# Kernel optimization log

Hardware: AMD Instinct MI355X
Metric: run time of the kernel (lower is better)

Reference implementation:

```python
import jax, jax.numpy as jnp
import numpy as np

N_WAY = 2
K_SHOT = 5
C = 320
NPTS = 2048
NQ = 2
K_PROTO = 100  # hardcoded k=100 in forward
N_CLS = N_WAY + 1
SIGMA = 1.0
NEG = -1e9


def _l2norm(x, eps=1e-8):
    return x / (jnp.linalg.norm(x, axis=-1, keepdims=True) + eps)


def _class_prototypes(feat, mask, k):
    """Multi-prototype masked pooling for one class.
    feat: [M, C] point features; mask: [M] float (1 = belongs to class).
    Picks k masked seed points, assigns every masked point to its
    nearest (cosine) seed, and returns the k masked cluster means.
    """
    M = feat.shape[0]
    # deterministic seeds: first k masked points (tie-break by index)
    score = mask - jnp.arange(M, dtype=feat.dtype) * 1e-9
    _, seed_idx = jax.lax.top_k(score, k)
    seeds = feat[seed_idx]                      # [k, C]
    sim = _l2norm(feat) @ _l2norm(seeds).T      # [M, k]
    assign = jnp.argmax(sim, axis=1)            # [M]
    onehot = jax.nn.one_hot(assign, k, dtype=feat.dtype) * mask[:, None]  # [M, k]
    num = onehot.T @ feat                       # [k, C]
    den = onehot.sum(axis=0)[:, None] + 1e-8
    return num / den


def _fg_prototypes(support_feat, fg_mask, k):
    # support_feat [n_way, k_shot, C, N] -> per-class point sets [n_way, k_shot*N, C]
    feat = support_feat.transpose(0, 1, 3, 2).reshape(N_WAY, -1, C)
    m = fg_mask.reshape(N_WAY, -1).astype(feat.dtype)
    protos = jax.vmap(lambda f, mm: _class_prototypes(f, mm, k))(feat, m)  # [n_way, k, C]
    labels = jnp.repeat(jnp.arange(1, N_WAY + 1), k)                        # classes 1..n_way
    return protos.reshape(-1, C), jax.nn.one_hot(labels, N_CLS, dtype=feat.dtype)


def _bg_prototypes(support_feat, bg_mask, k):
    feat = support_feat.transpose(0, 1, 3, 2).reshape(-1, C)   # all shots pooled
    m = bg_mask.reshape(-1).astype(feat.dtype)
    protos = _class_prototypes(feat, m, k)                      # [k, C]
    labels = jnp.zeros((k,), dtype=jnp.int32)                   # class 0 = background
    return protos, jax.nn.one_hot(labels, N_CLS, dtype=feat.dtype)


def _predict(prototypes, proto_onehot, qfeat, qlabels):
    # cosine similarity [M, P], per-class max over that class's prototypes
    sim = (_l2norm(qfeat) @ _l2norm(prototypes).T) / SIGMA        # [M, P]
    cls_mask = proto_onehot.T[None] > 0                            # [1, ncls, P]
    pred = jnp.max(jnp.where(cls_mask, sim[:, None, :], NEG), axis=-1)  # [M, ncls]
    logp = jax.nn.log_softmax(pred, axis=-1)
    loss = -jnp.mean(jnp.take_along_axis(logp, qlabels.reshape(-1, 1), axis=1))
    query_pred = pred.reshape(NQ, NPTS, N_CLS).transpose(0, 2, 1)  # [NQ, ncls, NPTS]
    return loss, query_pred


def reference(support_feat, query_feat, support_y, query_y):
    fg_mask = support_y
    bg_mask = 1 - support_y
    fg_protos, fg_labels = _fg_prototypes(support_feat, fg_mask, K_PROTO)
    bg_protos, bg_labels = _bg_prototypes(support_feat, bg_mask, K_PROTO)
    prototypes = jnp.concatenate([bg_protos, fg_protos], axis=0)           # [P, C]
    proto_labels = jnp.concatenate([bg_labels, fg_labels], axis=0)         # [P, ncls]

    qfeat = query_feat.transpose(0, 2, 1).reshape(-1, C)                   # [NQ*NPTS, C]
    loss, query_pred = _predict(prototypes, proto_labels, qfeat, query_y)
    # the forward adds computeCrossEntropyLoss(query_pred, query_y): same CE again
    loss = loss * 2.0

    # post-hoc per-point confidence thresholding (vectorized Python loop)
    qp = jnp.concatenate([query_pred[0], query_pred[1]], axis=-1)          # [ncls, NQ*NPTS]
    predictions = jnp.argmax(qp, axis=0)
    confidences = jnp.max(qp, axis=0)
    final = jnp.where(confidences > jnp.mean(confidences), predictions, -1)
    final_labels = jnp.stack([final[:NPTS], final[NPTS:]], axis=0)         # [2, NPTS]
    return loss, query_pred, final_labels


def setup_inputs() -> dict:
    key = jax.random.key(0)
    k1, k2, k3, k4 = jax.random.split(key, 4)
    return {
        "support_feat": jax.random.normal(k1, (N_WAY, K_SHOT, C, NPTS), dtype=jnp.float32),
        "query_feat": jax.random.normal(k2, (NQ, C, NPTS), dtype=jnp.float32),
        "support_y": jax.random.randint(k3, (N_WAY, K_SHOT, NPTS), 0, 2, dtype=jnp.int32),
        "query_y": jax.random.randint(k4, (NQ, NPTS), 0, 3, dtype=jnp.int32),
    }
```

## Files before the change

### kernel.cpp

```cpp
#include <hip/hip_runtime.h>
#include <math.h>

#define C 320
#define NPTS 2048
#define SUPPTS 20480
#define QPTS 4096
#define KP 100
#define NCLS 3
#define PSTRIDE 300

__global__ __launch_bounds__(64) void k_protoseed(const float* __restrict__ sup,
                                                  const int* __restrict__ sy,
                                                  float* __restrict__ pbufT) {
    int p    = blockIdx.x;
    int lane = threadIdx.x;
    int prob = (p < 100) ? 2 : ((p < 200) ? 0 : 1);
    int rank = (p < 100) ? p : ((p < 200) ? p - 100 : p - 200);
    int M    = (prob == 2) ? SUPPTS : 10240;
    int base = (prob == 1) ? 10240 : 0;
    int found = 0, sp = 0;
    for (int chunk = 0; chunk < M; chunk += 64) {
        int yy = sy[base + chunk + lane];
        int m  = (prob == 2) ? (1 - yy) : yy;
        unsigned long long bal = __ballot(m != 0);
        int cnt = __popcll(bal);
        if (found + cnt > rank) {
            int need = rank - found;
            int prefix = __popcll(bal & ((1ull << lane) - 1ull));
            unsigned long long match = __ballot(m && (prefix == need));
            int pos = __ffsll((unsigned long long)match) - 1;
            sp = base + chunk + pos;
            break;
        }
        found += cnt;
    }
    const float* fb = sup + ((size_t)(sp >> 11) * C) * NPTS + (sp & 2047);
    float v[5]; float s = 0.f;
    #pragma unroll
    for (int i = 0; i < 5; i++) {
        v[i] = fb[(size_t)(lane + i * 64) * NPTS];
        s += v[i] * v[i];
    }
    #pragma unroll
    for (int off = 32; off > 0; off >>= 1) s += __shfl_down(s, off);
    s = __shfl(s, 0);
    float r = 1.0f / (sqrtf(s) + 1e-8f);
    #pragma unroll
    for (int i = 0; i < 5; i++)
        pbufT[(size_t)(lane + i * 64) * PSTRIDE + p] = v[i] * r;
}

__global__ __launch_bounds__(256) void k_assign(const float* __restrict__ sup,
                                                const int* __restrict__ sy,
                                                const float* __restrict__ pbT,
                                                float* __restrict__ pmaxv,
                                                int* __restrict__ pmaxj) {
    __shared__ float shp[2 * C * 12 + 16];
    int b = blockIdx.x, jt = blockIdx.y, tid = threadIdx.x;
    int w = (b >= 40) ? 1 : 0;
    int colf = 100 + w * 100 + jt * 10;
    int colb = jt * 10;
    const int BGOFF = C * 12 + 16;
    for (int i = tid; i < C * 10; i += 256) {
        int c = i / 10, j = i % 10;
        shp[c * 12 + j]         = pbT[(size_t)c * PSTRIDE + colf + j];
        shp[BGOFF + c * 12 + j] = pbT[(size_t)c * PSTRIDE + colb + j];
    }
    int g = b * 256 + tid;
    int sel = sy[g] ? 0 : BGOFF;
    __syncthreads();
    const float* fb = sup + ((size_t)(g >> 11) * C) * NPTS + (g & 2047);
    float acc[10];
    #pragma unroll
    for (int j = 0; j < 10; j++) acc[j] = 0.f;
    float pf[8];
    #pragma unroll
    for (int k = 0; k < 8; k++) pf[k] = fb[(size_t)k * NPTS];
    for (int cc = 0; cc < C; cc += 8) {
        float cur[8];
        #pragma unroll
        for (int k = 0; k < 8; k++) cur[k] = pf[k];
        if (cc + 8 < C) {
            #pragma unroll
            for (int k = 0; k < 8; k++) pf[k] = fb[(size_t)(cc + 8 + k) * NPTS];
        }
        #pragma unroll
        for (int k = 0; k < 8; k++) {
            const float* row = &shp[sel + (cc + k) * 12];
            float4 p0 = ((const float4*)row)[0];
            float4 p1 = ((const float4*)row)[1];
            float2 p2 = *(const float2*)(row + 8);
            float px = cur[k];
            acc[0] += px * p0.x; acc[1] += px * p0.y;
            acc[2] += px * p0.z; acc[3] += px * p0.w;
            acc[4] += px * p1.x; acc[5] += px * p1.y;
            acc[6] += px * p1.z; acc[7] += px * p1.w;
            acc[8] += px * p2.x; acc[9] += px * p2.y;
        }
    }
    float bv = acc[0]; int bj = 0;
    #pragma unroll
    for (int j = 1; j < 10; j++) {
        if (acc[j] > bv) { bv = acc[j]; bj = j; }
    }
    size_t a0 = (size_t)jt * 20480 + g;
    pmaxv[a0] = bv;
    pmaxj[a0] = jt * 10 + bj;
}

__global__ __launch_bounds__(256) void k_combine_dst(const float* __restrict__ pmaxv,
                                                     const int* __restrict__ pmaxj,
                                                     const int* __restrict__ sy,
                                                     int* __restrict__ dst,
                                                     float* __restrict__ loss) {
    int g = blockIdx.x * 256 + threadIdx.x;
    if (g == 0) loss[0] = 0.f;
    if (g == 1) loss[1] = 0.f;
    float bv = pmaxv[g]; int bj = pmaxj[g];
    #pragma unroll
    for (int t = 1; t < 10; t++) {
        float v = pmaxv[(size_t)t * 20480 + g];
        if (v > bv) { bv = v; bj = pmaxj[(size_t)t * 20480 + g]; }
    }
    int way = (g >= 10240) ? 1 : 0;
    dst[g] = sy[g] ? (100 + way * 100 + bj) : bj;
}

__global__ __launch_bounds__(256) void k_accum_lds(const float* __restrict__ sup,
                                                   const int* __restrict__ dst,
                                                   float* __restrict__ part,
                                                   float* __restrict__ cnt) {
    __shared__ float bins[8 * 800];
    __shared__ float scnt[800];
    int bx = blockIdx.x;
    int ct = blockIdx.y;
    int tid = threadIdx.x;
    int copy = tid & 3;
    int ws = bx >> 1, half = bx & 1;
    int w = (ws >= 5) ? 1 : 0;
    int nbase = half * 1024;
    for (int i = tid; i < 8 * 800; i += 256) bins[i] = 0.f;
    if (ct == 0) { for (int i = tid; i < 800; i += 256) scnt[i] = 0.f; }
    int dreg[4];
    #pragma unroll
    for (int sub = 0; sub < 4; sub++) {
        int d = dst[ws * 2048 + nbase + sub * 256 + tid];
        dreg[sub] = (d < 100) ? d : (d - w * 100);
    }
    __syncthreads();
    if (ct == 0) {
        #pragma unroll
        for (int sub = 0; sub < 4; sub++) atomicAdd(&scnt[copy * 200 + dreg[sub]], 1.0f);
    }
    const float* base = sup + ((size_t)ws * C + ct * 8) * NPTS + nbase;
    for (int cl = 0; cl < 8; cl++) {
        const float* row = base + (size_t)cl * NPTS;
        #pragma unroll
        for (int sub = 0; sub < 4; sub++)
            atomicAdd(&bins[cl * 800 + copy * 200 + dreg[sub]], row[sub * 256 + tid]);
    }
    __syncthreads();
    float* pout = part + (size_t)(bx * 40 + ct) * 1600;
    for (int i = tid; i < 8 * 200; i += 256) {
        int bin = i >> 3, cl = i & 7;
        float s = bins[cl * 800 + bin] + bins[cl * 800 + 200 + bin]
                + bins[cl * 800 + 400 + bin] + bins[cl * 800 + 600 + bin];
        pout[i] = s;
    }
    if (ct == 0 && tid < 200)
        cnt[bx * 200 + tid] = scnt[tid] + scnt[200 + tid] + scnt[400 + tid] + scnt[600 + tid];
}

__global__ __launch_bounds__(64) void k_reduce_proto(const float* __restrict__ part,
                                                     const float* __restrict__ cnt,
                                                     float* __restrict__ phatT) {
    int d   = blockIdx.x;
    int tid = threadIdx.x;
    int local, s0, ns;
    if (d < 100)      { local = d;       s0 = 0;  ns = 20; }
    else if (d < 200) { local = d;       s0 = 0;  ns = 10; }
    else              { local = d - 100; s0 = 10; ns = 10; }
    float dn = 0.f;
    for (int k = 0; k < ns; k++) dn += cnt[(s0 + k) * 200 + local];
    float inv = 1.0f / (dn + 1e-8f);
    float vals[5]; float sq = 0.f;
    #pragma unroll
    for (int i = 0; i < 5; i++) {
        int c = tid + i * 64;
        int ct = c >> 3, cl = c & 7;
        float s = 0.f;
        for (int k = 0; k < ns; k++)
            s += part[(size_t)((s0 + k) * 40 + ct) * 1600 + local * 8 + cl];
        float v = s * inv;
        vals[i] = v; sq += v * v;
    }
    #pragma unroll
    for (int off = 32; off > 0; off >>= 1) sq += __shfl_down(sq, off);
    sq = __shfl(sq, 0);
    float rn = 1.0f / (sqrtf(sq) + 1e-8f);
    #pragma unroll
    for (int i = 0; i < 5; i++)
        phatT[(size_t)(tid + i * 64) * PSTRIDE + d] = vals[i] * rn;
}

__global__ __launch_bounds__(256) void k_qpartial(const float* __restrict__ qry,
                                                  const float* __restrict__ phT,
                                                  float* __restrict__ qmaxv,
                                                  float* __restrict__ qrn) {
    __shared__ float shp[C * 16];
    __shared__ float red[3 * 64 * 45];
    int pb = blockIdx.x, jt = blockIdx.y, tid = threadIdx.x;
    int wave = tid >> 6, lane = tid & 63;
    int j0 = jt * 10;
    for (int i = tid; i < C * 10; i += 256) {
        int j = i % 10, c = i / 10;
        shp[c * 16 + j] = phT[(size_t)c * PSTRIDE + j0 + j];
    }
    __syncthreads();
    int m = pb * 256 + lane * 4;
    int c0 = wave * 80;
    const float* fb = qry + ((size_t)(m >> 11) * C + c0) * NPTS + (m & 2047);
    float acc[4][10];
    #pragma unroll
    for (int p = 0; p < 4; p++)
        #pragma unroll
        for (int j = 0; j < 10; j++) acc[p][j] = 0.f;
    float qn[4] = {0.f, 0.f, 0.f, 0.f};
    float4 pf[8];
    #pragma unroll
    for (int k = 0; k < 8; k++) pf[k] = *(const float4*)(fb + (size_t)k * NPTS);
    for (int cc = 0; cc < 80; cc += 8) {
        float4 cur[8];
        #pragma unroll
        for (int k = 0; k < 8; k++) cur[k] = pf[k];
        if (cc + 8 < 80) {
            #pragma unroll
            for (int k = 0; k < 8; k++) pf[k] = *(const float4*)(fb + (size_t)(cc + 8 + k) * NPTS);
        }
        #pragma unroll
        for (int k = 0; k < 8; k++) {
            const float* row = &shp[(c0 + cc + k) * 16];
            float4 p0 = ((const float4*)row)[0];
            float4 p1 = ((const float4*)row)[1];
            float2 p2 = ((const float2*)row)[4];
            float pr[10] = {p0.x,p0.y,p0.z,p0.w,p1.x,p1.y,p1.z,p1.w,p2.x,p2.y};
            float4 cv = cur[k];
            if (jt == 0) {
                qn[0] += cv.x*cv.x; qn[1] += cv.y*cv.y; qn[2] += cv.z*cv.z; qn[3] += cv.w*cv.w;
            }
            #pragma unroll
            for (int j = 0; j < 10; j++) {
                acc[0][j] += cv.x * pr[j];
                acc[1][j] += cv.y * pr[j];
                acc[2][j] += cv.z * pr[j];
                acc[3][j] += cv.w * pr[j];
            }
        }
    }
    if (wave > 0) {
        float* my = red + ((wave - 1) * 64 + lane) * 45;
        #pragma unroll
        for (int p = 0; p < 4; p++)
            #pragma unroll
            for (int j = 0; j < 10; j++) my[p * 10 + j] = acc[p][j];
        #pragma unroll
        for (int p = 0; p < 4; p++) my[40 + p] = qn[p];
    }
    __syncthreads();
    if (wave == 0) {
        #pragma unroll
        for (int w = 0; w < 3; w++) {
            const float* my = red + (w * 64 + lane) * 45;
            #pragma unroll
            for (int p = 0; p < 4; p++)
                #pragma unroll
                for (int j = 0; j < 10; j++) acc[p][j] += my[p * 10 + j];
            #pragma unroll
            for (int p = 0; p < 4; p++) qn[p] += my[40 + p];
        }
        #pragma unroll
        for (int p = 0; p < 4; p++) {
            float bv = acc[p][0];
            #pragma unroll
            for (int j = 1; j < 10; j++) bv = fmaxf(bv, acc[p][j]);
            qmaxv[(size_t)(m + p) * 30 + jt] = bv;
        }
        if (jt == 0) {
            #pragma unroll
            for (int p = 0; p < 4; p++) qrn[m + p] = 1.0f / (sqrtf(qn[p]) + 1e-8f);
        }
    }
}

__global__ __launch_bounds__(256) void k_pred(const float* __restrict__ qmaxv,
                                              const float* __restrict__ qrn,
                                              const int* __restrict__ qy,
                                              float* __restrict__ out,
                                              float* __restrict__ lossacc,
                                              float* __restrict__ cbuf,
                                              int* __restrict__ lbuf) {
    __shared__ float redL[256];
    __shared__ float redC[256];
    int tid = threadIdx.x;
    int m = blockIdx.x * 256 + tid;
    float rn = qrn[m];
    float pred[NCLS];
    #pragma unroll
    for (int cls = 0; cls < NCLS; cls++) {
        float g = qmaxv[(size_t)m * 30 + cls * 10];
        #pragma unroll
        for (int t = 1; t < 10; t++) g = fmaxf(g, qmaxv[(size_t)m * 30 + cls * 10 + t]);
        pred[cls] = rn * g;
    }
    int q = m >> 11, n = m & 2047;
    #pragma unroll
    for (int cls = 0; cls < NCLS; cls++)
        out[1 + ((size_t)(q * NCLS + cls)) * NPTS + n] = pred[cls];
    float mx = fmaxf(pred[0], fmaxf(pred[1], pred[2]));
    float lse = mx + logf(expf(pred[0] - mx) + expf(pred[1] - mx) + expf(pred[2] - mx));
    int lab = 0; float cf = pred[0];
    if (pred[1] > cf) { cf = pred[1]; lab = 1; }
    if (pred[2] > cf) { cf = pred[2]; lab = 2; }
    cbuf[m] = cf; lbuf[m] = lab;
    redL[tid] = lse - pred[qy[m]];
    redC[tid] = cf;
    __syncthreads();
    for (int off = 128; off > 0; off >>= 1) {
        if (tid < off) { redL[tid] += redL[tid + off]; redC[tid] += redC[tid + off]; }
        __syncthreads();
    }
    if (tid == 0) {
        atomicAdd(&lossacc[0], redL[0]);
        atomicAdd(&lossacc[1], redC[0]);
    }
}

__global__ __launch_bounds__(256) void k_final(const float* __restrict__ cbuf,
                                               const int* __restrict__ lbuf,
                                               const float* __restrict__ lossacc,
                                               float* __restrict__ out) {
    int m = blockIdx.x * 256 + threadIdx.x;
    float mean = lossacc[1] / (float)QPTS;
    float cf = cbuf[m];
    out[1 + 2 * NCLS * NPTS + m] = (cf > mean) ? (float)lbuf[m] : -1.0f;
    if (m == 0) out[0] = 2.0f * lossacc[0] / (float)QPTS;
}

extern "C" void kernel_launch(void* const* d_in, const int* in_sizes, int n_in,
                              void* d_out, int out_size, void* d_ws, size_t ws_size,
                              hipStream_t stream) {
    const float* sup = (const float*)d_in[0];
    const float* qry = (const float*)d_in[1];
    const int*   sy  = (const int*)d_in[2];
    const int*   qy  = (const int*)d_in[3];
    float* out = (float*)d_out;

    float* f      = (float*)d_ws;
    float* qrn    = f;
    float* cnt    = qrn + QPTS;
    float* pbufT  = cnt + 4000;
    float* phatT  = pbufT + 96000;
    float* loss   = phatT + 96000;
    int*   dstb   = (int*)(loss + 4);
    float* trans  = (float*)(dstb + SUPPTS);
    float* pmaxv  = trans;
    int*   pmaxj  = (int*)(pmaxv + 204800);
    float* part   = trans;
    float* qmaxv  = trans;
    float* cbuf   = qmaxv + 122880;
    int*   lbuf   = (int*)(cbuf + QPTS);

    k_protoseed<<<300, 64, 0, stream>>>(sup, sy, pbufT);
    {
        dim3 grid(80, 10);
        k_assign<<<grid, 256, 0, stream>>>(sup, sy, pbufT, pmaxv, pmaxj);
    }
    k_combine_dst<<<80, 256, 0, stream>>>(pmaxv, pmaxj, sy, dstb, loss);
    {
        dim3 grid(20, 40);
        k_accum_lds<<<grid, 256, 0, stream>>>(sup, dstb, part, cnt);
    }
    k_reduce_proto<<<300, 64, 0, stream>>>(part, cnt, phatT);
    {
        dim3 grid(16, 30);
        k_qpartial<<<grid, 256, 0, stream>>>(qry, phatT, qmaxv, qrn);
    }
    k_pred<<<16, 256, 0, stream>>>(qmaxv, qrn, qy, out, loss, cbuf, lbuf);
    k_final<<<16, 256, 0, stream>>>(cbuf, lbuf, loss, out);
}
```

Measured before the change: 227.4 us.

## Restructure prototype accumulation with per-wave LDS bins and global cluster counts

Cluster counts are now built with global integer atomics in the combine kernel instead of LDS float counters in the accumulation kernel. The accumulation kernel now uses one bin copy per wave laid out as 16 channels per point group, with software-prefetched loads. It uses readlane checks to choose a plain LDS add when the four point groups hit distinct bins, and an atomic add otherwise. The goal is to cut LDS atomic contention and halve the grid, at the cost of strided 4-element global loads and extra global atomics.

```diff
diff --git a/kernel.cpp b/kernel.cpp
--- a/kernel.cpp
+++ b/kernel.cpp
@@ -11,9 +11,11 @@
 
 __global__ __launch_bounds__(64) void k_protoseed(const float* __restrict__ sup,
                                                   const int* __restrict__ sy,
-                                                  float* __restrict__ pbufT) {
+                                                  float* __restrict__ pbufT,
+                                                  int* __restrict__ cntG) {
     int p    = blockIdx.x;
     int lane = threadIdx.x;
+    if (lane == 0) cntG[p] = 0;
     int prob = (p < 100) ? 2 : ((p < 200) ? 0 : 1);
     int rank = (p < 100) ? p : ((p < 200) ? p - 100 : p - 200);
     int M    = (prob == 2) ? SUPPTS : 10240;
@@ -112,7 +114,8 @@
                                                      const int* __restrict__ pmaxj,
                                                      const int* __restrict__ sy,
                                                      int* __restrict__ dst,
-                                                     float* __restrict__ loss) {
+                                                     float* __restrict__ loss,
+                                                     int* __restrict__ cntG) {
     int g = blockIdx.x * 256 + threadIdx.x;
     if (g == 0) loss[0] = 0.f;
     if (g == 1) loss[1] = 0.f;
@@ -123,56 +126,70 @@
         if (v > bv) { bv = v; bj = pmaxj[(size_t)t * 20480 + g]; }
     }
     int way = (g >= 10240) ? 1 : 0;
-    dst[g] = sy[g] ? (100 + way * 100 + bj) : bj;
+    int dv = sy[g] ? (100 + way * 100 + bj) : bj;
+    dst[g] = dv;
+    atomicAdd(&cntG[dv], 1);
 }
 
 __global__ __launch_bounds__(256) void k_accum_lds(const float* __restrict__ sup,
                                                    const int* __restrict__ dst,
-                                                   float* __restrict__ part,
-                                                   float* __restrict__ cnt) {
-    __shared__ float bins[8 * 800];
-    __shared__ float scnt[800];
+                                                   float* __restrict__ part) {
+    __shared__ float bins[4 * 200 * 16];
+    __shared__ int   dl[1024];
     int bx = blockIdx.x;
-    int ct = blockIdx.y;
+    int by = blockIdx.y;
     int tid = threadIdx.x;
-    int copy = tid & 3;
     int ws = bx >> 1, half = bx & 1;
-    int w = (ws >= 5) ? 1 : 0;
-    int nbase = half * 1024;
-    for (int i = tid; i < 8 * 800; i += 256) bins[i] = 0.f;
-    if (ct == 0) { for (int i = tid; i < 800; i += 256) scnt[i] = 0.f; }
-    int dreg[4];
-    #pragma unroll
-    for (int sub = 0; sub < 4; sub++) {
-        int d = dst[ws * 2048 + nbase + sub * 256 + tid];
-        dreg[sub] = (d < 100) ? d : (d - w * 100);
-    }
-    __syncthreads();
-    if (ct == 0) {
-        #pragma unroll
-        for (int sub = 0; sub < 4; sub++) atomicAdd(&scnt[copy * 200 + dreg[sub]], 1.0f);
-    }
-    const float* base = sup + ((size_t)ws * C + ct * 8) * NPTS + nbase;
-    for (int cl = 0; cl < 8; cl++) {
-        const float* row = base + (size_t)cl * NPTS;
-        #pragma unroll
-        for (int sub = 0; sub < 4; sub++)
-            atomicAdd(&bins[cl * 800 + copy * 200 + dreg[sub]], row[sub * 256 + tid]);
-    }
-    __syncthreads();
-    float* pout = part + (size_t)(bx * 40 + ct) * 1600;
-    for (int i = tid; i < 8 * 200; i += 256) {
-        int bin = i >> 3, cl = i & 7;
-        float s = bins[cl * 800 + bin] + bins[cl * 800 + 200 + bin]
-                + bins[cl * 800 + 400 + bin] + bins[cl * 800 + 600 + bin];
-        pout[i] = s;
-    }
-    if (ct == 0 && tid < 200)
-        cnt[bx * 200 + tid] = scnt[tid] + scnt[200 + tid] + scnt[400 + tid] + scnt[600 + tid];
+    int wmask = (ws >= 5) ? 1 : 0;
+    int c0 = by * 16;
+
+    int4 d4 = *(const int4*)(dst + ws * 2048 + half * 1024 + 4 * tid);
+    dl[4 * tid + 0] = (d4.x < 100) ? d4.x : (d4.x - wmask * 100);
+    dl[4 * tid + 1] = (d4.y < 100) ? d4.y : (d4.y - wmask * 100);
+    dl[4 * tid + 2] = (d4.z < 100) ? d4.z : (d4.z - wmask * 100);
+    dl[4 * tid + 3] = (d4.w < 100) ? d4.w : (d4.w - wmask * 100);
+    for (int i = tid; i < 4 * 200 * 16; i += 256) bins[i] = 0.f;
+    __syncthreads();
+
+    int wv = tid >> 6, lane = tid & 63;
+    int ch = lane & 15, pq = lane >> 4;
+    float* mybins = bins + wv * 3200;
+    const int* dlp = dl + wv * 256 + pq;
+    const float* fb = sup + ((size_t)(ws * C + c0 + ch)) * NPTS + half * 1024 + wv * 256 + pq;
+
+    int   b_cur = dlp[0];
+    float f_cur = fb[0];
+    for (int it = 0; it < 64; it++) {
+        int nidx = (it < 63) ? (it + 1) * 4 : 0;
+        int   b_nxt = dlp[nidx];
+        float f_nxt = fb[nidx];
+        int b0 = __builtin_amdgcn_readlane(b_cur, 0);
+        int b1 = __builtin_amdgcn_readlane(b_cur, 16);
+        int b2 = __builtin_amdgcn_readlane(b_cur, 32);
+        int b3 = __builtin_amdgcn_readlane(b_cur, 48);
+        bool dup = (b0 == b1) | (b0 == b2) | (b0 == b3) |
+                   (b1 == b2) | (b1 == b3) | (b2 == b3);
+        int addr = b_cur * 16 + ch;
+        if (!dup) {
+            mybins[addr] += f_cur;
+        } else {
+            unsafeAtomicAdd(&mybins[addr], f_cur);
+        }
+        b_cur = b_nxt; f_cur = f_nxt;
+    }
+    __syncthreads();
+
+    for (int i = tid; i < 3200; i += 256) {
+        int bin = i >> 4, c = i & 15;
+        float s = bins[bin * 16 + c] + bins[3200 + bin * 16 + c]
+                + bins[6400 + bin * 16 + c] + bins[9600 + bin * 16 + c];
+        int ct8 = by * 2 + (c >> 3);
+        part[(size_t)(bx * 40 + ct8) * 1600 + bin * 8 + (c & 7)] = s;
+    }
 }
 
 __global__ __launch_bounds__(64) void k_reduce_proto(const float* __restrict__ part,
-                                                     const float* __restrict__ cnt,
+                                                     const int* __restrict__ cntG,
                                                      float* __restrict__ phatT) {
     int d   = blockIdx.x;
     int tid = threadIdx.x;
@@ -180,8 +197,7 @@
     if (d < 100)      { local = d;       s0 = 0;  ns = 20; }
     else if (d < 200) { local = d;       s0 = 0;  ns = 10; }
     else              { local = d - 100; s0 = 10; ns = 10; }
-    float dn = 0.f;
-    for (int k = 0; k < ns; k++) dn += cnt[(s0 + k) * 200 + local];
+    float dn = (float)cntG[d];
     float inv = 1.0f / (dn + 1e-8f);
     float vals[5]; float sq = 0.f;
     #pragma unroll
@@ -358,6 +374,7 @@
     float* f      = (float*)d_ws;
     float* qrn    = f;
     float* cnt    = qrn + QPTS;
+    int*   cntG   = (int*)cnt;
     float* pbufT  = cnt + 4000;
     float* phatT  = pbufT + 96000;
     float* loss   = phatT + 96000;
@@ -370,17 +387,17 @@
     float* cbuf   = qmaxv + 122880;
     int*   lbuf   = (int*)(cbuf + QPTS);
 
-    k_protoseed<<<300, 64, 0, stream>>>(sup, sy, pbufT);
+    k_protoseed<<<300, 64, 0, stream>>>(sup, sy, pbufT, cntG);
     {
         dim3 grid(80, 10);
         k_assign<<<grid, 256, 0, stream>>>(sup, sy, pbufT, pmaxv, pmaxj);
     }
-    k_combine_dst<<<80, 256, 0, stream>>>(pmaxv, pmaxj, sy, dstb, loss);
+    k_combine_dst<<<80, 256, 0, stream>>>(pmaxv, pmaxj, sy, dstb, loss, cntG);
     {
-        dim3 grid(20, 40);
-        k_accum_lds<<<grid, 256, 0, stream>>>(sup, dstb, part, cnt);
-    }
-    k_reduce_proto<<<300, 64, 0, stream>>>(part, cnt, phatT);
+        dim3 grid(20, 20);
+        k_accum_lds<<<grid, 256, 0, stream>>>(sup, dstb, part);
+    }
+    k_reduce_proto<<<300, 64, 0, stream>>>(part, cntG, phatT);
     {
         dim3 grid(16, 30);
         k_qpartial<<<grid, 256, 0, stream>>>(qry, phatT, qmaxv, qrn);
```

After: 203.2 us. 10.6% less time.
